# Performance work log

Measured on AMD Instinct MI355X. Metric: run time of the kernel, lower is better.

## Reference

```python
import jax, jax.numpy as jnp
import numpy as np

FILTERS = 256
KERNEL = 3
B, C, W = 8, 256, 8192
# he_std = gain / sqrt(fan_in) with fan_in = kernel_size * in_dim, lrmul = 1
RUNTIME_COEF = 1.0 / np.sqrt(KERNEL * C)


def setup_inputs() -> dict:
    key = jax.random.key(0)
    k1, k2, k3 = jax.random.split(key, 3)
    feature = jax.random.normal(k1, (B, C, W), dtype=jnp.float32)
    style = jax.random.normal(k2, (B, C), dtype=jnp.float32)
    kernel = jax.random.normal(k3, (KERNEL, C, FILTERS), dtype=jnp.float32)
    return {"feature": feature, "style": style, "kernel": kernel}


def reference(feature, style, kernel):
    b, c, w = feature.shape
    kk, _, f = kernel.shape
    # modulate: per-sample weights [B, k, C, F]
    weights = (kernel * RUNTIME_COEF)[None, ...] * (style[:, None, :, None] + 1.0)
    # demodulate: normalize over (k, C) per (B, F)
    denom = jax.lax.rsqrt(jnp.sum(jnp.square(weights), axis=(1, 2), keepdims=True))
    weights = weights * denom
    # batch-as-groups conv1d: lhs [1, B*C, W], rhs [k, C, B*F], groups = B
    lhs = feature.reshape(1, b * c, w)
    rhs = jnp.transpose(weights, (1, 2, 0, 3)).reshape(kk, c, b * f)
    out = jax.lax.conv_general_dilated(
        lhs, rhs,
        window_strides=(1,),
        padding="SAME",
        dimension_numbers=("NCH", "HIO", "NCH"),
        feature_group_count=b,
    )  # [1, B*F, W]
    return out.reshape(b, f, -1)
```

## Files before the change

### kernel.cpp

```cpp
#include <hip/hip_runtime.h>

#define B_   8
#define C_   256
#define W_   8192
#define F_   256
#define KK   3
#define KC   768
#define WP   (W_ + 2)
#define COEF 0.03608439182435161f
#define BK   64

using f32x16 = __attribute__((ext_vector_type(16))) float;
using bf16x8 = __attribute__((ext_vector_type(8))) __bf16;

#define AS1(p) ((const __attribute__((address_space(1))) void*)(p))
#define AS3(p) ((__attribute__((address_space(3))) void*)(p))

__device__ __forceinline__ unsigned short f2bf(float x) {
    union { float f; unsigned int u; } v; v.f = x;
    unsigned int u = v.u;
    u += 0x7FFFu + ((u >> 16) & 1u);
    return (unsigned short)(u >> 16);
}

__global__ void prep_kt(const float* __restrict__ kern, unsigned short* __restrict__ kT,
                        unsigned short* __restrict__ featT) {
    int idx = blockIdx.x * 256 + threadIdx.x;
    int f  = idx & 255;
    int kc = idx >> 8;
    kT[(size_t)f * KC + kc] = f2bf(kern[idx] * COEF);
    if (idx < 4096) {
        int b = idx >> 9, r = (idx >> 8) & 1, c = idx & 255;
        size_t row = r ? (size_t)(WP - 1) : 0;
        featT[((size_t)b * WP + row) * C_ + c] = 0;
    }
}

__global__ __launch_bounds__(256) void prep_denom(const float* __restrict__ kern,
                                                  const float* __restrict__ style,
                                                  float* __restrict__ denom) {
    __shared__ float sst[C_];
    const int b = blockIdx.x, f = threadIdx.x;
    sst[f] = (style[b * C_ + f] + 1.0f) * COEF;
    __syncthreads();
    float sum = 0.f;
#pragma unroll 8
    for (int kc = 0; kc < KC; ++kc) {
        float w = kern[(size_t)kc * F_ + f] * sst[kc & 255];
        sum += w * w;
    }
    denom[b * F_ + f] = rsqrtf(sum);
}

__global__ __launch_bounds__(256) void prep_featT(const float* __restrict__ feat,
                                                  const float* __restrict__ style,
                                                  unsigned short* __restrict__ featT) {
    __shared__ float tile[64][65];
    const int tid = threadIdx.x;
    const int b = blockIdx.z, c0 = blockIdx.y * 64, w0 = blockIdx.x * 64;

    const int x4 = tid & 15, cl4 = tid >> 4;
#pragma unroll
    for (int p = 0; p < 4; ++p) {
        const int cl = cl4 + p * 16;
        const float s = style[b * C_ + c0 + cl] + 1.0f;
        float4 v = *(const float4*)(feat + ((size_t)b * C_ + c0 + cl) * W_ + w0 + x4 * 4);
        tile[x4 * 4 + 0][cl] = v.x * s;
        tile[x4 * 4 + 1][cl] = v.y * s;
        tile[x4 * 4 + 2][cl] = v.z * s;
        tile[x4 * 4 + 3][cl] = v.w * s;
    }
    __syncthreads();

    const int ch = tid & 7, wr = tid >> 3;
#pragma unroll
    for (int p = 0; p < 2; ++p) {
        const int w = wr + p * 32;
        unsigned int pk[4];
#pragma unroll
        for (int j = 0; j < 4; ++j) {
            float v0 = tile[w][ch * 8 + 2 * j];
            float v1 = tile[w][ch * 8 + 2 * j + 1];
            pk[j] = (unsigned int)f2bf(v0) | ((unsigned int)f2bf(v1) << 16);
        }
        uint4 u; u.x = pk[0]; u.y = pk[1]; u.z = pk[2]; u.w = pk[3];
        *(uint4*)(featT + ((size_t)b * WP + (w0 + w + 1)) * C_ + c0 + ch * 8) = u;
    }
}

__global__ __launch_bounds__(256) void conv_mod(
        const unsigned short* __restrict__ featT,
        const unsigned short* __restrict__ kT,
        const float* __restrict__ denom,
        float* __restrict__ out) {
    __shared__ unsigned short As[128 * BK];
    __shared__ unsigned short Bs[128 * BK];

    const int tid  = threadIdx.x;
    const int b    = blockIdx.z;
    const int f0   = blockIdx.y * 128;
    const int w0   = blockIdx.x * 128;
    const int lane = tid & 63, wave = tid >> 6;
    const int wm   = (wave >> 1) * 64;
    const int wn   = (wave & 1) * 64;
    const int la   = lane & 31, kq = lane >> 5;

    const int lrow = lane >> 3, lchk = lane & 7, lswz = lchk ^ lrow;
    const unsigned short* asrc[4];
    const unsigned short* bsrc[4];
    int aldb[4], bldb[4];
#pragma unroll
    for (int i = 0; i < 4; ++i) {
        const int r = wave * 32 + i * 8;
        asrc[i] = kT + (size_t)(f0 + r + lrow) * KC + lswz * 8;
        bsrc[i] = featT + ((size_t)b * WP + (w0 + r + lrow)) * C_ + lswz * 8;
        aldb[i] = r * BK;
        bldb[i] = r * BK;
    }

    int aoff[2][4], boff[2][4];
#pragma unroll
    for (int mi = 0; mi < 2; ++mi) {
        const int row = wm + mi * 32 + la;
#pragma unroll
        for (int kh = 0; kh < 4; ++kh)
            aoff[mi][kh] = row * BK + ((kh * 2 + kq) ^ (la & 7)) * 8;
    }
#pragma unroll
    for (int ni = 0; ni < 2; ++ni) {
        const int row = wn + ni * 32 + la;
#pragma unroll
        for (int kh = 0; kh < 4; ++kh)
            boff[ni][kh] = row * BK + ((kh * 2 + kq) ^ (la & 7)) * 8;
    }

    f32x16 acc[2][2] = {};

    for (int it = 0; it < 12; ++it) {
        const int kc0 = it * 64;
        __syncthreads();
#pragma unroll
        for (int i = 0; i < 4; ++i) {
            __builtin_amdgcn_global_load_lds(AS1(asrc[i] + kc0), AS3(&As[aldb[i]]), 16, 0, 0);
            __builtin_amdgcn_global_load_lds(AS1(bsrc[i] + kc0), AS3(&Bs[bldb[i]]), 16, 0, 0);
        }
        __syncthreads();
#pragma unroll
        for (int kh = 0; kh < 4; ++kh) {
            bf16x8 a0 = *(const bf16x8*)&As[aoff[0][kh]];
            bf16x8 a1 = *(const bf16x8*)&As[aoff[1][kh]];
            bf16x8 b0 = *(const bf16x8*)&Bs[boff[0][kh]];
            bf16x8 b1 = *(const bf16x8*)&Bs[boff[1][kh]];
            acc[0][0] = __builtin_amdgcn_mfma_f32_32x32x16_bf16(a0, b0, acc[0][0], 0, 0, 0);
            acc[0][1] = __builtin_amdgcn_mfma_f32_32x32x16_bf16(a0, b1, acc[0][1], 0, 0, 0);
            acc[1][0] = __builtin_amdgcn_mfma_f32_32x32x16_bf16(a1, b0, acc[1][0], 0, 0, 0);
            acc[1][1] = __builtin_amdgcn_mfma_f32_32x32x16_bf16(a1, b1, acc[1][1], 0, 0, 0);
        }
    }

    const int bofs = b * F_;
    float* obase = out + (size_t)0;
#pragma unroll
    for (int mi = 0; mi < 2; ++mi) {
#pragma unroll
        for (int r = 0; r < 16; ++r) {
            const int frow = (r & 3) + 8 * (r >> 2) + 4 * kq;
            const int f = f0 + wm + mi * 32 + frow;
            const float d = denom[bofs + f];
            float* orow = obase + (size_t)(bofs + f) * W_ + w0 + wn + la;
            orow[0]  = acc[mi][0][r] * d;
            orow[32] = acc[mi][1][r] * d;
        }
    }
}

extern "C" void kernel_launch(void* const* d_in, const int* in_sizes, int n_in,
                              void* d_out, int out_size, void* d_ws, size_t ws_size,
                              hipStream_t stream) {
    const float* feature = (const float*)d_in[0];
    const float* style   = (const float*)d_in[1];
    const float* kern    = (const float*)d_in[2];
    float* out = (float*)d_out;

    unsigned short* kT    = (unsigned short*)d_ws;
    float*          denom = (float*)((char*)d_ws + (size_t)F_ * KC * 2);
    unsigned short* featT = (unsigned short*)((char*)d_ws + (size_t)F_ * KC * 2 + 8192);

    hipLaunchKernelGGL(prep_kt,    dim3(KC),     dim3(256), 0, stream, kern, kT, featT);
    hipLaunchKernelGGL(prep_denom, dim3(B_),     dim3(256), 0, stream, kern, style, denom);
    hipLaunchKernelGGL(prep_featT, dim3(W_ / 64, C_ / 64, B_), dim3(256), 0, stream,
                       feature, style, featT);
    hipLaunchKernelGGL(conv_mod,   dim3(W_ / 128, F_ / 128, B_), dim3(256), 0, stream,
                       featT, kT, denom, out);
}
```

Measured before the change: 175.7 us.

## Widen conv tile to all filters and double-buffer LDS loads with prefetch

The conv kernel now has each block compute all 256 filters for a 128-wide window, so each feature tile is loaded once instead of twice. The K step drops from 64 to 32, and the LDS tiles are double-buffered so the next slice's async global-to-LDS loads overlap the MFMAs on the current slice, with one barrier per iteration. Each wave now holds 8 accumulator tiles, which raises register pressure; launch bounds ask for 2 blocks per CU. The grid shrinks to half as many blocks.

Result: slower. 184.1 us (+4.8%).

```diff
diff --git a/kernel.cpp b/kernel.cpp
--- a/kernel.cpp
+++ b/kernel.cpp
@@ -8,7 +8,8 @@
 #define KC   768
 #define WP   (W_ + 2)
 #define COEF 0.03608439182435161f
-#define BK   64
+#define BK   32
+#define NIT  24
 
 using f32x16 = __attribute__((ext_vector_type(16))) float;
 using bf16x8 = __attribute__((ext_vector_type(8))) __bf16;
@@ -88,88 +89,107 @@
     }
 }
 
-__global__ __launch_bounds__(256) void conv_mod(
+__global__ __launch_bounds__(256, 2) void conv_mod(
         const unsigned short* __restrict__ featT,
         const unsigned short* __restrict__ kT,
         const float* __restrict__ denom,
         float* __restrict__ out) {
-    __shared__ unsigned short As[128 * BK];
-    __shared__ unsigned short Bs[128 * BK];
+    __shared__ unsigned short As[2 * 256 * BK];
+    __shared__ unsigned short Bs[2 * 128 * BK];
 
     const int tid  = threadIdx.x;
     const int b    = blockIdx.z;
-    const int f0   = blockIdx.y * 128;
     const int w0   = blockIdx.x * 128;
     const int lane = tid & 63, wave = tid >> 6;
-    const int wm   = (wave >> 1) * 64;
-    const int wn   = (wave & 1) * 64;
     const int la   = lane & 31, kq = lane >> 5;
 
-    const int lrow = lane >> 3, lchk = lane & 7, lswz = lchk ^ lrow;
-    const unsigned short* asrc[4];
-    const unsigned short* bsrc[4];
-    int aldb[4], bldb[4];
-#pragma unroll
-    for (int i = 0; i < 4; ++i) {
-        const int r = wave * 32 + i * 8;
-        asrc[i] = kT + (size_t)(f0 + r + lrow) * KC + lswz * 8;
-        bsrc[i] = featT + ((size_t)b * WP + (w0 + r + lrow)) * C_ + lswz * 8;
-        aldb[i] = r * BK;
-        bldb[i] = r * BK;
-    }
-
-    int aoff[2][4], boff[2][4];
-#pragma unroll
-    for (int mi = 0; mi < 2; ++mi) {
-        const int row = wm + mi * 32 + la;
-#pragma unroll
-        for (int kh = 0; kh < 4; ++kh)
-            aoff[mi][kh] = row * BK + ((kh * 2 + kq) ^ (la & 7)) * 8;
-    }
-#pragma unroll
-    for (int ni = 0; ni < 2; ++ni) {
-        const int row = wn + ni * 32 + la;
-#pragma unroll
-        for (int kh = 0; kh < 4; ++kh)
-            boff[ni][kh] = row * BK + ((kh * 2 + kq) ^ (la & 7)) * 8;
-    }
-
-    f32x16 acc[2][2] = {};
-
-    for (int it = 0; it < 12; ++it) {
-        const int kc0 = it * 64;
+    const int lrow = lane >> 2, lswz = (lane & 3) ^ (lrow & 3);
+    const unsigned short* asrc[4];  int aldb[4];
+    const unsigned short* bsrc[2];  int bldb[2];
+#pragma unroll
+    for (int j = 0; j < 4; ++j) {
+        const int r = wave * 64 + j * 16;
+        asrc[j] = kT + (size_t)(r + lrow) * KC + lswz * 8;
+        aldb[j] = r * BK;
+    }
+#pragma unroll
+    for (int j = 0; j < 2; ++j) {
+        const int r = wave * 32 + j * 16;
+        bsrc[j] = featT + ((size_t)b * WP + (w0 + r + lrow)) * C_ + lswz * 8;
+        bldb[j] = r * BK;
+    }
+
+    int ch[2];
+#pragma unroll
+    for (int s = 0; s < 2; ++s) ch[s] = ((s * 2 + kq) ^ (la & 3)) * 8;
+    int aoff[2][2], boff[4][2];
+#pragma unroll
+    for (int mi = 0; mi < 2; ++mi)
+#pragma unroll
+        for (int s = 0; s < 2; ++s)
+            aoff[mi][s] = (wave * 64 + mi * 32 + la) * BK + ch[s];
+#pragma unroll
+    for (int ni = 0; ni < 4; ++ni)
+#pragma unroll
+        for (int s = 0; s < 2; ++s)
+            boff[ni][s] = (ni * 32 + la) * BK + ch[s];
+
+    f32x16 acc[2][4] = {};
+
+#pragma unroll
+    for (int j = 0; j < 4; ++j)
+        __builtin_amdgcn_global_load_lds(AS1(asrc[j]), AS3(&As[aldb[j]]), 16, 0, 0);
+#pragma unroll
+    for (int j = 0; j < 2; ++j)
+        __builtin_amdgcn_global_load_lds(AS1(bsrc[j]), AS3(&Bs[bldb[j]]), 16, 0, 0);
+
+#pragma unroll 2
+    for (int it = 0; it < NIT; ++it) {
+        const int cur = (it & 1);
         __syncthreads();
-#pragma unroll
-        for (int i = 0; i < 4; ++i) {
-            __builtin_amdgcn_global_load_lds(AS1(asrc[i] + kc0), AS3(&As[aldb[i]]), 16, 0, 0);
-            __builtin_amdgcn_global_load_lds(AS1(bsrc[i] + kc0), AS3(&Bs[bldb[i]]), 16, 0, 0);
-        }
-        __syncthreads();
-#pragma unroll
-        for (int kh = 0; kh < 4; ++kh) {
-            bf16x8 a0 = *(const bf16x8*)&As[aoff[0][kh]];
-            bf16x8 a1 = *(const bf16x8*)&As[aoff[1][kh]];
-            bf16x8 b0 = *(const bf16x8*)&Bs[boff[0][kh]];
-            bf16x8 b1 = *(const bf16x8*)&Bs[boff[1][kh]];
-            acc[0][0] = __builtin_amdgcn_mfma_f32_32x32x16_bf16(a0, b0, acc[0][0], 0, 0, 0);
-            acc[0][1] = __builtin_amdgcn_mfma_f32_32x32x16_bf16(a0, b1, acc[0][1], 0, 0, 0);
-            acc[1][0] = __builtin_amdgcn_mfma_f32_32x32x16_bf16(a1, b0, acc[1][0], 0, 0, 0);
-            acc[1][1] = __builtin_amdgcn_mfma_f32_32x32x16_bf16(a1, b1, acc[1][1], 0, 0, 0);
+        if (it + 1 < NIT) {
+            const int nxt = cur ^ 1;
+            const int kc = (it + 1) * BK;
+#pragma unroll
+            for (int j = 0; j < 4; ++j)
+                __builtin_amdgcn_global_load_lds(AS1(asrc[j] + kc),
+                                                 AS3(&As[nxt * 256 * BK + aldb[j]]), 16, 0, 0);
+#pragma unroll
+            for (int j = 0; j < 2; ++j)
+                __builtin_amdgcn_global_load_lds(AS1(bsrc[j] + kc),
+                                                 AS3(&Bs[nxt * 128 * BK + bldb[j]]), 16, 0, 0);
+        }
+        const unsigned short* Ab = &As[cur * 256 * BK];
+        const unsigned short* Bb = &Bs[cur * 128 * BK];
+#pragma unroll
+        for (int s = 0; s < 2; ++s) {
+            bf16x8 aF[2], bF[4];
+#pragma unroll
+            for (int mi = 0; mi < 2; ++mi) aF[mi] = *(const bf16x8*)&Ab[aoff[mi][s]];
+#pragma unroll
+            for (int ni = 0; ni < 4; ++ni) bF[ni] = *(const bf16x8*)&Bb[boff[ni][s]];
+#pragma unroll
+            for (int mi = 0; mi < 2; ++mi)
+#pragma unroll
+                for (int ni = 0; ni < 4; ++ni)
+                    acc[mi][ni] = __builtin_amdgcn_mfma_f32_32x32x16_bf16(
+                        aF[mi], bF[ni], acc[mi][ni], 0, 0, 0);
         }
     }
 
     const int bofs = b * F_;
-    float* obase = out + (size_t)0;
 #pragma unroll
     for (int mi = 0; mi < 2; ++mi) {
 #pragma unroll
         for (int r = 0; r < 16; ++r) {
             const int frow = (r & 3) + 8 * (r >> 2) + 4 * kq;
-            const int f = f0 + wm + mi * 32 + frow;
+            const int f = wave * 64 + mi * 32 + frow;
             const float d = denom[bofs + f];
-            float* orow = obase + (size_t)(bofs + f) * W_ + w0 + wn + la;
+            float* orow = out + (size_t)(bofs + f) * W_ + w0 + la;
             orow[0]  = acc[mi][0][r] * d;
             orow[32] = acc[mi][1][r] * d;
+            orow[64] = acc[mi][2][r] * d;
+            orow[96] = acc[mi][3][r] * d;
         }
     }
 }
@@ -190,6 +210,6 @@
     hipLaunchKernelGGL(prep_denom, dim3(B_),     dim3(256), 0, stream, kern, style, denom);
     hipLaunchKernelGGL(prep_featT, dim3(W_ / 64, C_ / 64, B_), dim3(256), 0, stream,
                        feature, style, featT);
-    hipLaunchKernelGGL(conv_mod,   dim3(W_ / 128, F_ / 128, B_), dim3(256), 0, stream,
+    hipLaunchKernelGGL(conv_mod,   dim3(W_ / 128, 1, B_), dim3(256), 0, stream,
                        featT, kT, denom, out);
 }
```
